# Performance work log

Measured on AMD Instinct MI355X. Metric: run time of the kernel, lower is better.

Reference implementation:

```python
import jax, jax.numpy as jnp
import numpy as np

PROJ_SCALE = 0.1


def setup_inputs() -> dict:
    key = jax.random.key(0)
    ks = jax.random.split(key, 6)
    B, D, K, E = 8192, 256, 63, 64  # batch, n_features, num_breakpoints, emb_dim_per_feature
    x_num = jax.random.normal(ks[0], (B, D), dtype=jnp.float32)
    basis_weight = jax.random.normal(ks[1], (D, K + 1, E), dtype=jnp.float32) * 0.001
    basis_bias = jnp.zeros((D, E), dtype=jnp.float32)
    proj_w = jax.random.normal(ks[2], (D, D * E), dtype=jnp.float32) * 0.01  # torch Linear weight (out, in)
    proj_b = jnp.zeros((D,), dtype=jnp.float32)
    breakpoint_min = jax.random.normal(ks[3], (D, 1), dtype=jnp.float32) * 0.1
    breakpoint_delta_raw = jax.random.normal(ks[4], (D, K), dtype=jnp.float32) * 0.5
    return {
        "x_num": x_num,
        "basis_weight": basis_weight,
        "basis_bias": basis_bias,
        "proj_w": proj_w,
        "proj_b": proj_b,
        "breakpoint_min": breakpoint_min,
        "breakpoint_delta_raw": breakpoint_delta_raw,
    }


def reference(x_num, basis_weight, basis_bias, proj_w, proj_b, breakpoint_min, breakpoint_delta_raw):
    # breakpoints: monotone via softplus deltas + cumsum, shape [D, K]
    deltas = jax.nn.softplus(breakpoint_delta_raw)
    breakpoints = breakpoint_min + jnp.cumsum(deltas, axis=1)
    # piecewise-linear basis: [B, D, K+1]
    basis = jax.nn.relu(x_num[:, :, None] - breakpoints[None, :, :])
    basis = jnp.concatenate([x_num[:, :, None], basis], axis=-1)
    # per-feature batched matmul: [B, D, E]
    embeddings = jnp.einsum("bdf,dfe->bde", basis, basis_weight) + basis_bias
    flat = embeddings.reshape(x_num.shape[0], -1)  # [B, D*E]
    x_emb = x_num + PROJ_SCALE * (flat @ proj_w.T + proj_b)
    return x_emb, embeddings, breakpoints
```

## Files before the change

kernel.cpp:

```cpp
#include <hip/hip_runtime.h>
#include <hip/hip_bf16.h>

#define NB 8192
#define ND 256
#define NKBP 63
#define NF 64
#define NE 64
#define NKP 16384
#define NDE 16384
#define NSPLIT 4

typedef __attribute__((ext_vector_type(8))) short short8_t;
typedef __attribute__((ext_vector_type(4))) short short4_t;
typedef __attribute__((ext_vector_type(4))) float f32x4;

__device__ __forceinline__ unsigned short bfbits(float v) {
  union { __hip_bfloat16 b; unsigned short u; } cv;
  cv.b = __float2bfloat16(v);
  return cv.u;
}
__device__ __forceinline__ float bf2f(unsigned short s) {
  return __uint_as_float(((unsigned)s) << 16);
}

__global__ void k_maxx(const float* __restrict__ x, float* __restrict__ bmax) {
  const int t = threadIdx.x;
  const float* px = x + (size_t)blockIdx.x * 8192;
  float m = 0.f;
  #pragma unroll 4
  for (int i = t; i < 8192; i += 256) m = fmaxf(m, px[i]);
  #pragma unroll
  for (int off = 32; off > 0; off >>= 1) m = fmaxf(m, __shfl_down(m, off, 64));
  __shared__ float red[4];
  if ((t & 63) == 0) red[t >> 6] = m;
  __syncthreads();
  if (t == 0) bmax[blockIdx.x] = fmaxf(fmaxf(red[0], red[1]), fmaxf(red[2], red[3]));
}

__global__ void k_bp(const float* __restrict__ bmin, const float* __restrict__ draw,
                     const float* __restrict__ bmax, float* __restrict__ obp,
                     int* __restrict__ fdv, int* __restrict__ fcutc,
                     float* __restrict__ thrT) {
  const int d = threadIdx.x;
  __shared__ float mred[256];
  __shared__ int fds[256];
  mred[d] = bmax[d];
  __syncthreads();
  for (int s = 128; s > 0; s >>= 1) {
    if (d < s) mred[d] = fmaxf(mred[d], mred[d + s]);
    __syncthreads();
  }
  const float maxx = mred[0];
  float a = bmin[d];
  int cnt = 0;
  if (thrT) thrT[d * 64] = 0.0f;
  for (int j = 0; j < NKBP; ++j) {
    float r = draw[d * NKBP + j];
    a += fmaxf(r, 0.f) + log1pf(expf(-fabsf(r)));
    obp[d * NKBP + j] = a;
    if (thrT) thrT[d * 64 + 1 + j] = a;
    cnt += (a < maxx) ? 1 : 0;
  }
  const int Fd = 1 + cnt;
  fdv[d] = Fd;
  fds[d] = Fd;
  __syncthreads();
  if (d < NSPLIT) {
    int mx = 0;
    for (int k = 0; k < 64; ++k) mx = max(mx, fds[d * 64 + k]);
    fcutc[d] = (mx > 32) ? 2 : 1;
  }
}

__global__ void k_prep(const float* __restrict__ bw, unsigned short* __restrict__ bwT) {
  const int d = blockIdx.x;
  const int t = threadIdx.x;
  const int f = t >> 2, e0 = (t & 3) * 16;
  const int kf = f >> 5, lg = (f >> 3) & 3, j = f & 7;
  const size_t base = ((((size_t)d * 2 + kf) * 4 + lg) * 64) * 8 + j;
  #pragma unroll
  for (int q = 0; q < 4; ++q) {
    f32x4 v = *(const f32x4*)(bw + (size_t)d * 4096 + f * 64 + e0 + q * 4);
    #pragma unroll
    for (int r = 0; r < 4; ++r)
      bwT[base + (size_t)(e0 + q * 4 + r) * 8] = bfbits(v[r]);
  }
}

__global__ __launch_bounds__(256, 2) void k_w2(
    const float* __restrict__ bw, const float* __restrict__ pw,
    const float* __restrict__ bb, const int* __restrict__ fcutc,
    unsigned short* __restrict__ w2f, float* __restrict__ cb_part) {
  const int d = blockIdx.x;
  const int t = threadIdx.x;
  const int l = t & 63, w = t >> 6;
  const int lr = l & 15, lg = l >> 4;
  const int nkf = fcutc[d >> 6];
  __shared__ unsigned short pwS[256 * 72];
  __shared__ unsigned short bwS[64 * 72];
  __shared__ float bbS[64];

  {
    const int rr = t >> 4, e0 = (t & 15) * 4;
    #pragma unroll
    for (int it = 0; it < 16; ++it) {
      const int n = it * 16 + rr;
      f32x4 v = *(const f32x4*)(pw + (size_t)n * NDE + d * 64 + e0);
      short4_t s;
      s[0] = (short)bfbits(v[0]); s[1] = (short)bfbits(v[1]);
      s[2] = (short)bfbits(v[2]); s[3] = (short)bfbits(v[3]);
      *(short4_t*)(pwS + n * 72 + e0) = s;
    }
    const int itmax = (nkf == 2) ? 4 : 2;
    for (int it = 0; it < itmax; ++it) {
      const int f = it * 16 + rr;
      f32x4 v = *(const f32x4*)(bw + (size_t)d * 4096 + f * 64 + e0);
      short4_t s;
      s[0] = (short)bfbits(v[0]); s[1] = (short)bfbits(v[1]);
      s[2] = (short)bfbits(v[2]); s[3] = (short)bfbits(v[3]);
      *(short4_t*)(bwS + f * 72 + e0) = s;
    }
    if (t < 64) bbS[t] = bb[(size_t)d * 64 + t];
  }
  __syncthreads();

  f32x4 acc[4][4];
  #pragma unroll
  for (int mi = 0; mi < 4; ++mi)
    #pragma unroll
    for (int ni = 0; ni < 4; ++ni) acc[mi][ni] = (f32x4){0.f, 0.f, 0.f, 0.f};

  const int nimax = (nkf == 2) ? 4 : 2;
  for (int kf = 0; kf < nkf; ++kf) {
    short8_t afr[4], bfr[4];
    #pragma unroll
    for (int mi = 0; mi < 4; ++mi) {
      const int n = w * 64 + mi * 16 + lr;
      afr[mi] = *(const short8_t*)(pwS + n * 72 + kf * 32 + lg * 8);
    }
    for (int ni = 0; ni < nimax; ++ni) {
      const int f = ni * 16 + lr;
      bfr[ni] = *(const short8_t*)(bwS + f * 72 + kf * 32 + lg * 8);
    }
    for (int ni = 0; ni < nimax; ++ni)
      #pragma unroll
      for (int mi = 0; mi < 4; ++mi)
        acc[mi][ni] = __builtin_amdgcn_mfma_f32_16x16x32_bf16(afr[mi], bfr[ni], acc[mi][ni], 0, 0, 0);
  }

  #pragma unroll
  for (int mi = 0; mi < 4; ++mi)
    for (int ni = 0; ni < nimax; ++ni) {
      const int kf_s = ni >> 1;
      const int lgp  = (ni * 2 + (lr >> 3)) & 3;
      const int jj   = lr & 7;
      const int nb   = w * 64 + mi * 16 + lg * 4;
      const size_t base = (((size_t)d * 2 + kf_s) * 4 + lgp) * 256;
      #pragma unroll
      for (int r = 0; r < 4; ++r)
        w2f[(base + (nb + r)) * 8 + jj] = bfbits(acc[mi][ni][r]);
    }

  {
    float cacc = 0.f;
    #pragma unroll 8
    for (int e = 0; e < 64; ++e) cacc += bf2f(pwS[t * 72 + e]) * bbS[e];
    cb_part[(size_t)d * 256 + t] = cacc;
  }
}

__global__ void k_cbr(const float* __restrict__ cb_part, float* __restrict__ c) {
  const int t = threadIdx.x;
  float a0 = 0.f, a1 = 0.f, a2 = 0.f, a3 = 0.f;
  for (int d = 0; d < ND; d += 4) {
    a0 += cb_part[(size_t)(d + 0) * 256 + t];
    a1 += cb_part[(size_t)(d + 1) * 256 + t];
    a2 += cb_part[(size_t)(d + 2) * 256 + t];
    a3 += cb_part[(size_t)(d + 3) * 256 + t];
  }
  c[t] = (a0 + a1) + (a2 + a3);
}

template<bool KF1>
__device__ __forceinline__ void proj_kloop(
    const unsigned short* const (&bbase)[4], const float* const (&xrow)[2],
    const float* thrS_lg, bool lg0, f32x4 (&acc)[2][4]) {
  for (int c = 0; c < 8; ++c) {
    f32x4 xqa[2], xqb[2];
    #pragma unroll
    for (int mi = 0; mi < 2; ++mi) {
      xqa[mi] = *(const f32x4*)(xrow[mi] + c * 8);
      xqb[mi] = *(const f32x4*)(xrow[mi] + c * 8 + 4);
    }
    #pragma unroll
    for (int dd = 0; dd < 8; ++dd) {
      const int dl = c * 8 + dd;
      short8_t bfr0[4], bfr1[4];
      #pragma unroll
      for (int ni = 0; ni < 4; ++ni)
        bfr0[ni] = *(const short8_t*)(bbase[ni] + (size_t)dl * 16384);
      if (KF1) {
        #pragma unroll
        for (int ni = 0; ni < 4; ++ni)
          bfr1[ni] = *(const short8_t*)(bbase[ni] + (size_t)dl * 16384 + 8192);
      }
      const float* tp = thrS_lg + dl * 64;
      f32x4 ta = *(const f32x4*)(tp);
      f32x4 tb = *(const f32x4*)(tp + 4);
      short8_t afr0[2], afr1[2];
      #pragma unroll
      for (int mi = 0; mi < 2; ++mi) {
        const float xv = (dd < 4) ? xqa[mi][dd & 3] : xqb[mi][dd & 3];
        short8_t A0;
        A0[0] = (short)bfbits(lg0 ? xv : fmaxf(xv - ta[0], 0.f));
        A0[1] = (short)bfbits(fmaxf(xv - ta[1], 0.f));
        A0[2] = (short)bfbits(fmaxf(xv - ta[2], 0.f));
        A0[3] = (short)bfbits(fmaxf(xv - ta[3], 0.f));
        A0[4] = (short)bfbits(fmaxf(xv - tb[0], 0.f));
        A0[5] = (short)bfbits(fmaxf(xv - tb[1], 0.f));
        A0[6] = (short)bfbits(fmaxf(xv - tb[2], 0.f));
        A0[7] = (short)bfbits(fmaxf(xv - tb[3], 0.f));
        afr0[mi] = A0;
      }
      if (KF1) {
        f32x4 tc = *(const f32x4*)(tp + 32);
        f32x4 td = *(const f32x4*)(tp + 36);
        #pragma unroll
        for (int mi = 0; mi < 2; ++mi) {
          const float xv = (dd < 4) ? xqa[mi][dd & 3] : xqb[mi][dd & 3];
          short8_t A1;
          A1[0] = (short)bfbits(fmaxf(xv - tc[0], 0.f));
          A1[1] = (short)bfbits(fmaxf(xv - tc[1], 0.f));
          A1[2] = (short)bfbits(fmaxf(xv - tc[2], 0.f));
          A1[3] = (short)bfbits(fmaxf(xv - tc[3], 0.f));
          A1[4] = (short)bfbits(fmaxf(xv - td[0], 0.f));
          A1[5] = (short)bfbits(fmaxf(xv - td[1], 0.f));
          A1[6] = (short)bfbits(fmaxf(xv - td[2], 0.f));
          A1[7] = (short)bfbits(fmaxf(xv - td[3], 0.f));
          afr1[mi] = A1;
        }
      }
      #pragma unroll
      for (int mi = 0; mi < 2; ++mi)
        #pragma unroll
        for (int ni = 0; ni < 4; ++ni)
          acc[mi][ni] = __builtin_amdgcn_mfma_f32_16x16x32_bf16(afr0[mi], bfr0[ni], acc[mi][ni], 0, 0, 0);
      if (KF1) {
        #pragma unroll
        for (int mi = 0; mi < 2; ++mi)
          #pragma unroll
          for (int ni = 0; ni < 4; ++ni)
            acc[mi][ni] = __builtin_amdgcn_mfma_f32_16x16x32_bf16(afr1[mi], bfr1[ni], acc[mi][ni], 0, 0, 0);
      }
    }
  }
}

__global__ __launch_bounds__(256, 3) void k_proj(
    const unsigned short* __restrict__ w2f, const float* __restrict__ bp,
    const float* __restrict__ x, const int* __restrict__ fcutc,
    float* __restrict__ pbuf) {
  const int t = threadIdx.x;
  const int l = t & 63, w = t >> 6;
  const int lr = l & 15, lg = l >> 4;
  const int bM = blockIdx.x * 128;
  const int bN = blockIdx.y * 64;
  const int d0 = blockIdx.z * 64;
  __shared__ float thrS[64 * 64];

  for (int i = t; i < 4096; i += 256) {
    const int dl = i >> 6, f = i & 63;
    thrS[i] = (f >= 1) ? bp[(size_t)(d0 + dl) * NKBP + f - 1] : 0.0f;
  }
  __syncthreads();

  f32x4 acc[2][4];
  #pragma unroll
  for (int mi = 0; mi < 2; ++mi)
    #pragma unroll
    for (int ni = 0; ni < 4; ++ni) acc[mi][ni] = (f32x4){0.f, 0.f, 0.f, 0.f};

  const bool lg0 = (lg == 0);
  const unsigned short* bbase[4];
  #pragma unroll
  for (int ni = 0; ni < 4; ++ni)
    bbase[ni] = w2f + (size_t)d0 * 16384 + (size_t)(bN + ni * 16 + lr) * 8 + (size_t)lg * 2048;
  const float* xrow[2];
  #pragma unroll
  for (int mi = 0; mi < 2; ++mi)
    xrow[mi] = x + (size_t)(bM + w * 32 + mi * 16 + lr) * ND + d0;

  const int nkf = fcutc[blockIdx.z];
  if (nkf == 1) proj_kloop<false>(bbase, xrow, thrS + lg * 8, lg0, acc);
  else          proj_kloop<true >(bbase, xrow, thrS + lg * 8, lg0, acc);

  float* pp = pbuf + (size_t)blockIdx.z * ((size_t)NB * ND);
  #pragma unroll
  for (int mi = 0; mi < 2; ++mi)
    #pragma unroll
    for (int ni = 0; ni < 4; ++ni) {
      const int col = bN + ni * 16 + lr;
      const int rowb = bM + w * 32 + mi * 16 + lg * 4;
      #pragma unroll
      for (int r = 0; r < 4; ++r)
        pp[(size_t)(rowb + r) * ND + col] = acc[mi][ni][r];
    }
}

__global__ void k_comb(const float* __restrict__ x, const float* __restrict__ pbuf,
                       const float* __restrict__ cbuf, const float* __restrict__ pb,
                       float* __restrict__ xe) {
  const size_t i = ((size_t)blockIdx.x * 256 + threadIdx.x) * 4;
  const int n = (int)(i & 255);
  f32x4 s = *(const f32x4*)(pbuf + i);
  #pragma unroll
  for (int p = 1; p < NSPLIT; ++p)
    s += *(const f32x4*)(pbuf + (size_t)p * 2097152 + i);
  f32x4 cv = *(const f32x4*)(cbuf + n);
  f32x4 pv = *(const f32x4*)(pb + n);
  f32x4 xv = *(const f32x4*)(x + i);
  *(f32x4*)(xe + i) = xv + 0.1f * (s + cv + pv);
}

__global__ __launch_bounds__(256, 3) void k_emb(
    const float* __restrict__ x, const unsigned short* __restrict__ bwT,
    const float* __restrict__ bb, const float* __restrict__ thrT,
    const int* __restrict__ fdv, float* __restrict__ oe) {
  const int d = blockIdx.x;
  const int b0 = blockIdx.y * 256;
  const int t = threadIdx.x;
  const int l = t & 63, w = t >> 6;
  const int lr = l & 15, lg = l >> 4;
  __shared__ float cS[4 * 32 * 68];

  const int nkf = (fdv[d] > 32) ? 2 : 1;

  float xg[4];
  #pragma unroll
  for (int mi = 0; mi < 4; ++mi)
    xg[mi] = x[(size_t)(b0 + w * 64 + mi * 16 + lr) * ND + d];

  f32x4 ta = *(const f32x4*)(thrT + d * 64 + lg * 8);
  f32x4 tb = *(const f32x4*)(thrT + d * 64 + lg * 8 + 4);
  const bool lg0 = (lg == 0);

  float bbv[4];
  #pragma unroll
  for (int ni = 0; ni < 4; ++ni) bbv[ni] = bb[(size_t)d * 64 + ni * 16 + lr];

  const unsigned short* bk0 = bwT + ((size_t)d * 8 + lg) * 512;
  short8_t bfr0[4];
  #pragma unroll
  for (int ni = 0; ni < 4; ++ni)
    bfr0[ni] = *(const short8_t*)(bk0 + (ni * 16 + lr) * 8);

  short8_t afr0[4];
  #pragma unroll
  for (int mi = 0; mi < 4; ++mi) {
    const float xv = xg[mi];
    short8_t A0;
    A0[0] = (short)bfbits(lg0 ? xv : fmaxf(xv - ta[0], 0.f));
    A0[1] = (short)bfbits(fmaxf(xv - ta[1], 0.f));
    A0[2] = (short)bfbits(fmaxf(xv - ta[2], 0.f));
    A0[3] = (short)bfbits(fmaxf(xv - ta[3], 0.f));
    A0[4] = (short)bfbits(fmaxf(xv - tb[0], 0.f));
    A0[5] = (short)bfbits(fmaxf(xv - tb[1], 0.f));
    A0[6] = (short)bfbits(fmaxf(xv - tb[2], 0.f));
    A0[7] = (short)bfbits(fmaxf(xv - tb[3], 0.f));
    afr0[mi] = A0;
  }

  f32x4 acc[4][4];
  #pragma unroll
  for (int mi = 0; mi < 4; ++mi)
    #pragma unroll
    for (int ni = 0; ni < 4; ++ni) acc[mi][ni] = (f32x4){0.f, 0.f, 0.f, 0.f};
  #pragma unroll
  for (int mi = 0; mi < 4; ++mi)
    #pragma unroll
    for (int ni = 0; ni < 4; ++ni)
      acc[mi][ni] = __builtin_amdgcn_mfma_f32_16x16x32_bf16(afr0[mi], bfr0[ni], acc[mi][ni], 0, 0, 0);

  if (nkf == 2) {
    f32x4 tc = *(const f32x4*)(thrT + d * 64 + 32 + lg * 8);
    f32x4 td = *(const f32x4*)(thrT + d * 64 + 36 + lg * 8);
    const unsigned short* bk1 = bwT + ((size_t)d * 8 + 4 + lg) * 512;
    short8_t afr1[4], bfr1[4];
    #pragma unroll
    for (int ni = 0; ni < 4; ++ni)
      bfr1[ni] = *(const short8_t*)(bk1 + (ni * 16 + lr) * 8);
    #pragma unroll
    for (int mi = 0; mi < 4; ++mi) {
      const float xv = xg[mi];
      short8_t A1;
      A1[0] = (short)bfbits(fmaxf(xv - tc[0], 0.f));
      A1[1] = (short)bfbits(fmaxf(xv - tc[1], 0.f));
      A1[2] = (short)bfbits(fmaxf(xv - tc[2], 0.f));
      A1[3] = (short)bfbits(fmaxf(xv - tc[3], 0.f));
      A1[4] = (short)bfbits(fmaxf(xv - td[0], 0.f));
      A1[5] = (short)bfbits(fmaxf(xv - td[1], 0.f));
      A1[6] = (short)bfbits(fmaxf(xv - td[2], 0.f));
      A1[7] = (short)bfbits(fmaxf(xv - td[3], 0.f));
      afr1[mi] = A1;
    }
    #pragma unroll
    for (int mi = 0; mi < 4; ++mi)
      #pragma unroll
      for (int ni = 0; ni < 4; ++ni)
        acc[mi][ni] = __builtin_amdgcn_mfma_f32_16x16x32_bf16(afr1[mi], bfr1[ni], acc[mi][ni], 0, 0, 0);
  }

  const int rsub = l >> 4;
  const int c4 = (l & 15) * 4;
  #pragma unroll
  for (int half = 0; half < 2; ++half) {
    #pragma unroll
    for (int ni = 0; ni < 4; ++ni) {
      #pragma unroll
      for (int mi = 0; mi < 2; ++mi) {
        const int rw = mi * 16 + lg * 4;
        #pragma unroll
        for (int r = 0; r < 4; ++r)
          cS[w * 2176 + (rw + r) * 68 + ni * 16 + lr] = acc[half * 2 + mi][ni][r] + bbv[ni];
      }
    }
    #pragma unroll
    for (int p = 0; p < 8; ++p) {
      const int rl = p * 4 + rsub;
      f32x4 v = *(const f32x4*)(cS + w * 2176 + rl * 68 + c4);
      *(f32x4*)(oe + (size_t)(b0 + w * 64 + half * 32 + rl) * NDE + d * 64 + c4) = v;
    }
  }
}

__global__ __launch_bounds__(256, 2) void k_emb_fb(
    const float* __restrict__ x, const float* __restrict__ bw,
    const float* __restrict__ bb, const float* __restrict__ bp,
    const int* __restrict__ fdv, float* __restrict__ oe) {
  const int d = blockIdx.x;
  const int b0 = blockIdx.y * 256;
  const int t = threadIdx.x;
  const int l = t & 63, w = t >> 6;
  const int lr = l & 15, lg = l >> 4;
  __shared__ unsigned short btS[64 * 72];
  __shared__ float thrF[64];
  __shared__ float bbS[64];
  __shared__ float cS[4 * 64 * 68];

  const int nkf = (fdv[d] > 32) ? 2 : 1;
  float xg[4];
  #pragma unroll
  for (int mi = 0; mi < 4; ++mi)
    xg[mi] = x[(size_t)(b0 + w * 64 + mi * 16 + lr) * ND + d];

  if (t < 64) thrF[t] = (t >= 1) ? bp[(size_t)d * NKBP + t - 1] : 0.0f;
  else if (t < 128) bbS[t - 64] = bb[(size_t)d * 64 + (t - 64)];
  {
    const float* bwd = bw + (size_t)d * 4096;
    const int f = t >> 2, e0 = (t & 3) * 16;
    #pragma unroll
    for (int q = 0; q < 4; ++q) {
      f32x4 v = *(const f32x4*)(bwd + f * 64 + e0 + q * 4);
      #pragma unroll
      for (int r = 0; r < 4; ++r) {
        const int e = e0 + q * 4 + r;
        btS[e * 72 + f] = bfbits(v[r]);
      }
    }
  }
  __syncthreads();

  f32x4 ta = *(const f32x4*)(thrF + lg * 8);
  f32x4 tb = *(const f32x4*)(thrF + lg * 8 + 4);
  const bool lg0 = (lg == 0);

  short8_t afr0[4];
  #pragma unroll
  for (int mi = 0; mi < 4; ++mi) {
    const float xv = xg[mi];
    short8_t A0;
    A0[0] = (short)bfbits(lg0 ? xv : fmaxf(xv - ta[0], 0.f));
    A0[1] = (short)bfbits(fmaxf(xv - ta[1], 0.f));
    A0[2] = (short)bfbits(fmaxf(xv - ta[2], 0.f));
    A0[3] = (short)bfbits(fmaxf(xv - ta[3], 0.f));
    A0[4] = (short)bfbits(fmaxf(xv - tb[0], 0.f));
    A0[5] = (short)bfbits(fmaxf(xv - tb[1], 0.f));
    A0[6] = (short)bfbits(fmaxf(xv - tb[2], 0.f));
    A0[7] = (short)bfbits(fmaxf(xv - tb[3], 0.f));
    afr0[mi] = A0;
  }
  short8_t bfr0[4];
  #pragma unroll
  for (int ni = 0; ni < 4; ++ni) {
    const int e = ni * 16 + lr;
    bfr0[ni] = *(const short8_t*)(btS + e * 72 + lg * 8);
  }
  f32x4 acc[4][4];
  #pragma unroll
  for (int mi = 0; mi < 4; ++mi)
    #pragma unroll
    for (int ni = 0; ni < 4; ++ni) acc[mi][ni] = (f32x4){0.f, 0.f, 0.f, 0.f};
  #pragma unroll
  for (int mi = 0; mi < 4; ++mi)
    #pragma unroll
    for (int ni = 0; ni < 4; ++ni)
      acc[mi][ni] = __builtin_amdgcn_mfma_f32_16x16x32_bf16(afr0[mi], bfr0[ni], acc[mi][ni], 0, 0, 0);

  if (nkf == 2) {
    f32x4 tc = *(const f32x4*)(thrF + 32 + lg * 8);
    f32x4 td = *(const f32x4*)(thrF + 36 + lg * 8);
    short8_t afr1[4], bfr1[4];
    #pragma unroll
    for (int mi = 0; mi < 4; ++mi) {
      const float xv = xg[mi];
      short8_t A1;
      A1[0] = (short)bfbits(fmaxf(xv - tc[0], 0.f));
      A1[1] = (short)bfbits(fmaxf(xv - tc[1], 0.f));
      A1[2] = (short)bfbits(fmaxf(xv - tc[2], 0.f));
      A1[3] = (short)bfbits(fmaxf(xv - tc[3], 0.f));
      A1[4] = (short)bfbits(fmaxf(xv - td[0], 0.f));
      A1[5] = (short)bfbits(fmaxf(xv - td[1], 0.f));
      A1[6] = (short)bfbits(fmaxf(xv - td[2], 0.f));
      A1[7] = (short)bfbits(fmaxf(xv - td[3], 0.f));
      afr1[mi] = A1;
    }
    #pragma unroll
    for (int ni = 0; ni < 4; ++ni) {
      const int e = ni * 16 + lr;
      bfr1[ni] = *(const short8_t*)(btS + e * 72 + 32 + lg * 8);
    }
    #pragma unroll
    for (int mi = 0; mi < 4; ++mi)
      #pragma unroll
      for (int ni = 0; ni < 4; ++ni)
        acc[mi][ni] = __builtin_amdgcn_mfma_f32_16x16x32_bf16(afr1[mi], bfr1[ni], acc[mi][ni], 0, 0, 0);
  }

  #pragma unroll
  for (int ni = 0; ni < 4; ++ni) {
    const float bbv = bbS[ni * 16 + lr];
    #pragma unroll
    for (int mi = 0; mi < 4; ++mi) {
      const int rw = mi * 16 + lg * 4;
      #pragma unroll
      for (int r = 0; r < 4; ++r)
        cS[w * 4352 + (rw + r) * 68 + ni * 16 + lr] = acc[mi][ni][r] + bbv;
    }
  }
  __syncthreads();

  const int rsub = t >> 4;
  const int c4 = (t & 15) * 4;
  #pragma unroll
  for (int p = 0; p < 16; ++p) {
    const int row = p * 16 + rsub;
    const int wsrc = row >> 6, wr = row & 63;
    f32x4 v = *(const f32x4*)(cS + wsrc * 4352 + wr * 68 + c4);
    *(f32x4*)(oe + (size_t)(b0 + row) * NDE + d * 64 + c4) = v;
  }
}

extern "C" void kernel_launch(void* const* d_in, const int* in_sizes, int n_in,
                              void* d_out, int out_size, void* d_ws, size_t ws_size,
                              hipStream_t stream) {
  const float* x    = (const float*)d_in[0];
  const float* bw   = (const float*)d_in[1];
  const float* bb   = (const float*)d_in[2];
  const float* pw   = (const float*)d_in[3];
  const float* pb   = (const float*)d_in[4];
  const float* bmin = (const float*)d_in[5];
  const float* draw = (const float*)d_in[6];

  float* out    = (float*)d_out;
  float* out_x  = out;
  float* out_e  = out + (size_t)NB * ND;
  float* out_bp = out_e + (size_t)NB * NDE;

  unsigned short* w2f = (unsigned short*)out_x;
  float* cbuf    = out_e;
  float* pbuf    = out_e + 65536;
  float* cb_part = out_e + 65536 + NSPLIT * 2097152;

  float* wsf  = (float*)d_ws;
  float* bmax = wsf;
  int*   fdv  = (int*)wsf + 256;
  int*   fcutc= (int*)wsf + 512;
  float* thrT = wsf + 768;
  unsigned short* bwT = (unsigned short*)(wsf + 768 + 16384);
  const bool FAST = ws_size >= (size_t)(768 + 16384) * 4 + (size_t)2097152 * 2 + 256;

  k_maxx<<<dim3(256),          dim3(256), 0, stream>>>(x, bmax);
  k_bp  <<<dim3(1),            dim3(256), 0, stream>>>(bmin, draw, bmax, out_bp, fdv, fcutc,
                                                       FAST ? thrT : (float*)nullptr);
  if (FAST)
    k_prep<<<dim3(256),        dim3(256), 0, stream>>>(bw, bwT);
  k_w2  <<<dim3(256),          dim3(256), 0, stream>>>(bw, pw, bb, fcutc, w2f, cb_part);
  k_cbr <<<dim3(1),            dim3(256), 0, stream>>>(cb_part, cbuf);
  k_proj<<<dim3(64, 4, NSPLIT),dim3(256), 0, stream>>>(w2f, out_bp, x, fcutc, pbuf);
  k_comb<<<dim3(2048),         dim3(256), 0, stream>>>(x, pbuf, cbuf, pb, out_x);
  if (FAST)
    k_emb <<<dim3(256, 32),    dim3(256), 0, stream>>>(x, bwT, bb, thrT, fdv, out_e);
  else
    k_emb_fb<<<dim3(256, 32),  dim3(256), 0, stream>>>(x, bw, bb, out_bp, fdv, out_e);
}
```

Baseline: 261.5 us.

## Restructure embedding kernel to write full contiguous output rows per batch tile

```diff
diff --git a/kernel.cpp b/kernel.cpp
--- a/kernel.cpp
+++ b/kernel.cpp
@@ -23,6 +23,32 @@
   return __uint_as_float(((unsigned)s) << 16);
 }
 
+__global__ void k_mp(const float* __restrict__ x, const float* __restrict__ bw,
+                     float* __restrict__ bmax, unsigned short* __restrict__ bwT) {
+  const int t = threadIdx.x;
+  const float* px = x + (size_t)blockIdx.x * 8192;
+  float m = 0.f;
+  #pragma unroll 4
+  for (int i = t; i < 8192; i += 256) m = fmaxf(m, px[i]);
+  #pragma unroll
+  for (int off = 32; off > 0; off >>= 1) m = fmaxf(m, __shfl_down(m, off, 64));
+  __shared__ float red[4];
+  if ((t & 63) == 0) red[t >> 6] = m;
+  __syncthreads();
+  if (t == 0) bmax[blockIdx.x] = fmaxf(fmaxf(red[0], red[1]), fmaxf(red[2], red[3]));
+  const int d = blockIdx.x;
+  const int f = t >> 2, e0 = (t & 3) * 16;
+  const int kf = f >> 5, lg = (f >> 3) & 3, j = f & 7;
+  const size_t base = ((((size_t)d * 2 + kf) * 4 + lg) * 64) * 8 + j;
+  #pragma unroll
+  for (int q = 0; q < 4; ++q) {
+    f32x4 v = *(const f32x4*)(bw + (size_t)d * 4096 + f * 64 + e0 + q * 4);
+    #pragma unroll
+    for (int r = 0; r < 4; ++r)
+      bwT[base + (size_t)(e0 + q * 4 + r) * 8] = bfbits(v[r]);
+  }
+}
+
 __global__ void k_maxx(const float* __restrict__ x, float* __restrict__ bmax) {
   const int t = threadIdx.x;
   const float* px = x + (size_t)blockIdx.x * 8192;
@@ -42,9 +68,11 @@
                      int* __restrict__ fdv, int* __restrict__ fcutc,
                      float* __restrict__ thrT) {
   const int d = threadIdx.x;
+  __shared__ float drawS[ND * NKBP];
   __shared__ float mred[256];
   __shared__ int fds[256];
   mred[d] = bmax[d];
+  for (int i = d; i < ND * NKBP; i += 256) drawS[i] = draw[i];
   __syncthreads();
   for (int s = 128; s > 0; s >>= 1) {
     if (d < s) mred[d] = fmaxf(mred[d], mred[d + s]);
@@ -55,7 +83,7 @@
   int cnt = 0;
   if (thrT) thrT[d * 64] = 0.0f;
   for (int j = 0; j < NKBP; ++j) {
-    float r = draw[d * NKBP + j];
+    float r = drawS[d * NKBP + j];
     a += fmaxf(r, 0.f) + log1pf(expf(-fabsf(r)));
     obp[d * NKBP + j] = a;
     if (thrT) thrT[d * 64 + 1 + j] = a;
@@ -69,21 +97,6 @@
     int mx = 0;
     for (int k = 0; k < 64; ++k) mx = max(mx, fds[d * 64 + k]);
     fcutc[d] = (mx > 32) ? 2 : 1;
-  }
-}
-
-__global__ void k_prep(const float* __restrict__ bw, unsigned short* __restrict__ bwT) {
-  const int d = blockIdx.x;
-  const int t = threadIdx.x;
-  const int f = t >> 2, e0 = (t & 3) * 16;
-  const int kf = f >> 5, lg = (f >> 3) & 3, j = f & 7;
-  const size_t base = ((((size_t)d * 2 + kf) * 4 + lg) * 64) * 8 + j;
-  #pragma unroll
-  for (int q = 0; q < 4; ++q) {
-    f32x4 v = *(const f32x4*)(bw + (size_t)d * 4096 + f * 64 + e0 + q * 4);
-    #pragma unroll
-    for (int r = 0; r < 4; ++r)
-      bwT[base + (size_t)(e0 + q * 4 + r) * 8] = bfbits(v[r]);
   }
 }
 
@@ -322,37 +335,131 @@
   *(f32x4*)(xe + i) = xv + 0.1f * (s + cv + pv);
 }
 
-__global__ __launch_bounds__(256, 3) void k_emb(
+__global__ __launch_bounds__(256, 2) void k_emb2(
     const float* __restrict__ x, const unsigned short* __restrict__ bwT,
     const float* __restrict__ bb, const float* __restrict__ thrT,
+    const int* __restrict__ fdv, const int* __restrict__ fcutc,
+    float* __restrict__ oe) {
+  const int b0 = blockIdx.x * 16;
+  const int t = threadIdx.x;
+  const int l = t & 63, w = t >> 6;
+  const int lr = l & 15, lg = l >> 4;
+  __shared__ float xS[16 * 260];
+  __shared__ float thrS[256 * 32];
+  __shared__ float slab[16 * 268];
+
+  {
+    const int r = t >> 4, c16 = (t & 15) * 16;
+    #pragma unroll
+    for (int q = 0; q < 4; ++q) {
+      f32x4 v = *(const f32x4*)(x + (size_t)(b0 + r) * ND + c16 + q * 4);
+      *(f32x4*)(xS + r * 260 + c16 + q * 4) = v;
+    }
+  }
+  for (int i = t; i < 256 * 32; i += 256) {
+    const int dS = i >> 5, f = i & 31;
+    thrS[i] = thrT[dS * 64 + f];
+  }
+  int fc[NSPLIT];
+  #pragma unroll
+  for (int z = 0; z < NSPLIT; ++z) fc[z] = fcutc[z];
+  __syncthreads();
+
+  const bool lg0 = (lg == 0);
+  const int ecol = w * 16 + lr;
+
+  for (int g = 0; g < 64; ++g) {
+    #pragma unroll
+    for (int dd = 0; dd < 4; ++dd) {
+      const int d = g * 4 + dd;
+      f32x4 ta = *(const f32x4*)(thrS + d * 32 + lg * 8);
+      f32x4 tb = *(const f32x4*)(thrS + d * 32 + lg * 8 + 4);
+      const float xv = xS[lr * 260 + d];
+      short8_t A0;
+      A0[0] = (short)bfbits(lg0 ? xv : fmaxf(xv - ta[0], 0.f));
+      A0[1] = (short)bfbits(fmaxf(xv - ta[1], 0.f));
+      A0[2] = (short)bfbits(fmaxf(xv - ta[2], 0.f));
+      A0[3] = (short)bfbits(fmaxf(xv - ta[3], 0.f));
+      A0[4] = (short)bfbits(fmaxf(xv - tb[0], 0.f));
+      A0[5] = (short)bfbits(fmaxf(xv - tb[1], 0.f));
+      A0[6] = (short)bfbits(fmaxf(xv - tb[2], 0.f));
+      A0[7] = (short)bfbits(fmaxf(xv - tb[3], 0.f));
+      short8_t B0 = *(const short8_t*)(bwT + ((size_t)d * 8 + lg) * 512 + ecol * 8);
+      const float bbv = bb[(size_t)d * 64 + ecol];
+      f32x4 acc = (f32x4){0.f, 0.f, 0.f, 0.f};
+      acc = __builtin_amdgcn_mfma_f32_16x16x32_bf16(A0, B0, acc, 0, 0, 0);
+      if (fc[d >> 6] == 2) {
+        if (fdv[d] > 32) {
+          f32x4 tc = *(const f32x4*)(thrT + d * 64 + 32 + lg * 8);
+          f32x4 td = *(const f32x4*)(thrT + d * 64 + 36 + lg * 8);
+          short8_t A1;
+          A1[0] = (short)bfbits(fmaxf(xv - tc[0], 0.f));
+          A1[1] = (short)bfbits(fmaxf(xv - tc[1], 0.f));
+          A1[2] = (short)bfbits(fmaxf(xv - tc[2], 0.f));
+          A1[3] = (short)bfbits(fmaxf(xv - tc[3], 0.f));
+          A1[4] = (short)bfbits(fmaxf(xv - td[0], 0.f));
+          A1[5] = (short)bfbits(fmaxf(xv - td[1], 0.f));
+          A1[6] = (short)bfbits(fmaxf(xv - td[2], 0.f));
+          A1[7] = (short)bfbits(fmaxf(xv - td[3], 0.f));
+          short8_t B1 = *(const short8_t*)(bwT + ((size_t)d * 8 + 4 + lg) * 512 + ecol * 8);
+          acc = __builtin_amdgcn_mfma_f32_16x16x32_bf16(A1, B1, acc, 0, 0, 0);
+        }
+      }
+      #pragma unroll
+      for (int r2 = 0; r2 < 4; ++r2)
+        slab[(lg * 4 + r2) * 268 + dd * 64 + ecol] = acc[r2] + bbv;
+    }
+    __syncthreads();
+    #pragma unroll
+    for (int rr = 0; rr < 4; ++rr) {
+      const int row = w * 4 + rr;
+      f32x4 v = *(const f32x4*)(slab + row * 268 + l * 4);
+      *(f32x4*)(oe + (size_t)(b0 + row) * NDE + g * 256 + l * 4) = v;
+    }
+    __syncthreads();
+  }
+}
+
+__global__ __launch_bounds__(256, 2) void k_emb_fb(
+    const float* __restrict__ x, const float* __restrict__ bw,
+    const float* __restrict__ bb, const float* __restrict__ bp,
     const int* __restrict__ fdv, float* __restrict__ oe) {
   const int d = blockIdx.x;
   const int b0 = blockIdx.y * 256;
   const int t = threadIdx.x;
   const int l = t & 63, w = t >> 6;
   const int lr = l & 15, lg = l >> 4;
-  __shared__ float cS[4 * 32 * 68];
+  __shared__ unsigned short btS[64 * 72];
+  __shared__ float thrF[64];
+  __shared__ float bbS[64];
+  __shared__ float cS[4 * 64 * 68];
 
   const int nkf = (fdv[d] > 32) ? 2 : 1;
-
   float xg[4];
   #pragma unroll
   for (int mi = 0; mi < 4; ++mi)
     xg[mi] = x[(size_t)(b0 + w * 64 + mi * 16 + lr) * ND + d];
 
-  f32x4 ta = *(const f32x4*)(thrT + d * 64 + lg * 8);
-  f32x4 tb = *(const f32x4*)(thrT + d * 64 + lg * 8 + 4);
+  if (t < 64) thrF[t] = (t >= 1) ? bp[(size_t)d * NKBP + t - 1] : 0.0f;
+  else if (t < 128) bbS[t - 64] = bb[(size_t)d * 64 + (t - 64)];
+  {
+    const float* bwd = bw + (size_t)d * 4096;
+    const int f = t >> 2, e0 = (t & 3) * 16;
+    #pragma unroll
+    for (int q = 0; q < 4; ++q) {
+      f32x4 v = *(const f32x4*)(bwd + f * 64 + e0 + q * 4);
+      #pragma unroll
+      for (int r = 0; r < 4; ++r) {
+        const int e = e0 + q * 4 + r;
+        btS[e * 72 + f] = bfbits(v[r]);
+      }
+    }
+  }
+  __syncthreads();
+
+  f32x4 ta = *(const f32x4*)(thrF + lg * 8);
+  f32x4 tb = *(const f32x4*)(thrF + lg * 8 + 4);
   const bool lg0 = (lg == 0);
-
-  float bbv[4];
-  #pragma unroll
-  for (int ni = 0; ni < 4; ++ni) bbv[ni] = bb[(size_t)d * 64 + ni * 16 + lr];
-
-  const unsigned short* bk0 = bwT + ((size_t)d * 8 + lg) * 512;
-  short8_t bfr0[4];
-  #pragma unroll
-  for (int ni = 0; ni < 4; ++ni)
-    bfr0[ni] = *(const short8_t*)(bk0 + (ni * 16 + lr) * 8);
 
   short8_t afr0[4];
   #pragma unroll
@@ -369,7 +476,12 @@
     A0[7] = (short)bfbits(fmaxf(xv - tb[3], 0.f));
     afr0[mi] = A0;
   }
-
+  short8_t bfr0[4];
+  #pragma unroll
+  for (int ni = 0; ni < 4; ++ni) {
+    const int e = ni * 16 + lr;
+    bfr0[ni] = *(const short8_t*)(btS + e * 72 + lg * 8);
+  }
   f32x4 acc[4][4];
   #pragma unroll
   for (int mi = 0; mi < 4; ++mi)
@@ -382,13 +494,9 @@
       acc[mi][ni] = __builtin_amdgcn_mfma_f32_16x16x32_bf16(afr0[mi], bfr0[ni], acc[mi][ni], 0, 0, 0);
 
   if (nkf == 2) {
-    f32x4 tc = *(const f32x4*)(thrT + d * 64 + 32 + lg * 8);
-    f32x4 td = *(const f32x4*)(thrT + d * 64 + 36 + lg * 8);
-    const unsigned short* bk1 = bwT + ((size_t)d * 8 + 4 + lg) * 512;
+    f32x4 tc = *(const f32x4*)(thrF + 32 + lg * 8);
+    f32x4 td = *(const f32x4*)(thrF + 36 + lg * 8);
     short8_t afr1[4], bfr1[4];
-    #pragma unroll
-    for (int ni = 0; ni < 4; ++ni)
-      bfr1[ni] = *(const short8_t*)(bk1 + (ni * 16 + lr) * 8);
     #pragma unroll
     for (int mi = 0; mi < 4; ++mi) {
       const float xv = xg[mi];
@@ -404,127 +512,6 @@
       afr1[mi] = A1;
     }
     #pragma unroll
-    for (int mi = 0; mi < 4; ++mi)
-      #pragma unroll
-      for (int ni = 0; ni < 4; ++ni)
-        acc[mi][ni] = __builtin_amdgcn_mfma_f32_16x16x32_bf16(afr1[mi], bfr1[ni], acc[mi][ni], 0, 0, 0);
-  }
-
-  const int rsub = l >> 4;
-  const int c4 = (l & 15) * 4;
-  #pragma unroll
-  for (int half = 0; half < 2; ++half) {
-    #pragma unroll
-    for (int ni = 0; ni < 4; ++ni) {
-      #pragma unroll
-      for (int mi = 0; mi < 2; ++mi) {
-        const int rw = mi * 16 + lg * 4;
-        #pragma unroll
-        for (int r = 0; r < 4; ++r)
-          cS[w * 2176 + (rw + r) * 68 + ni * 16 + lr] = acc[half * 2 + mi][ni][r] + bbv[ni];
-      }
-    }
-    #pragma unroll
-    for (int p = 0; p < 8; ++p) {
-      const int rl = p * 4 + rsub;
-      f32x4 v = *(const f32x4*)(cS + w * 2176 + rl * 68 + c4);
-      *(f32x4*)(oe + (size_t)(b0 + w * 64 + half * 32 + rl) * NDE + d * 64 + c4) = v;
-    }
-  }
-}
-
-__global__ __launch_bounds__(256, 2) void k_emb_fb(
-    const float* __restrict__ x, const float* __restrict__ bw,
-    const float* __restrict__ bb, const float* __restrict__ bp,
-    const int* __restrict__ fdv, float* __restrict__ oe) {
-  const int d = blockIdx.x;
-  const int b0 = blockIdx.y * 256;
-  const int t = threadIdx.x;
-  const int l = t & 63, w = t >> 6;
-  const int lr = l & 15, lg = l >> 4;
-  __shared__ unsigned short btS[64 * 72];
-  __shared__ float thrF[64];
-  __shared__ float bbS[64];
-  __shared__ float cS[4 * 64 * 68];
-
-  const int nkf = (fdv[d] > 32) ? 2 : 1;
-  float xg[4];
-  #pragma unroll
-  for (int mi = 0; mi < 4; ++mi)
-    xg[mi] = x[(size_t)(b0 + w * 64 + mi * 16 + lr) * ND + d];
-
-  if (t < 64) thrF[t] = (t >= 1) ? bp[(size_t)d * NKBP + t - 1] : 0.0f;
-  else if (t < 128) bbS[t - 64] = bb[(size_t)d * 64 + (t - 64)];
-  {
-    const float* bwd = bw + (size_t)d * 4096;
-    const int f = t >> 2, e0 = (t & 3) * 16;
-    #pragma unroll
-    for (int q = 0; q < 4; ++q) {
-      f32x4 v = *(const f32x4*)(bwd + f * 64 + e0 + q * 4);
-      #pragma unroll
-      for (int r = 0; r < 4; ++r) {
-        const int e = e0 + q * 4 + r;
-        btS[e * 72 + f] = bfbits(v[r]);
-      }
-    }
-  }
-  __syncthreads();
-
-  f32x4 ta = *(const f32x4*)(thrF + lg * 8);
-  f32x4 tb = *(const f32x4*)(thrF + lg * 8 + 4);
-  const bool lg0 = (lg == 0);
-
-  short8_t afr0[4];
-  #pragma unroll
-  for (int mi = 0; mi < 4; ++mi) {
-    const float xv = xg[mi];
-    short8_t A0;
-    A0[0] = (short)bfbits(lg0 ? xv : fmaxf(xv - ta[0], 0.f));
-    A0[1] = (short)bfbits(fmaxf(xv - ta[1], 0.f));
-    A0[2] = (short)bfbits(fmaxf(xv - ta[2], 0.f));
-    A0[3] = (short)bfbits(fmaxf(xv - ta[3], 0.f));
-    A0[4] = (short)bfbits(fmaxf(xv - tb[0], 0.f));
-    A0[5] = (short)bfbits(fmaxf(xv - tb[1], 0.f));
-    A0[6] = (short)bfbits(fmaxf(xv - tb[2], 0.f));
-    A0[7] = (short)bfbits(fmaxf(xv - tb[3], 0.f));
-    afr0[mi] = A0;
-  }
-  short8_t bfr0[4];
-  #pragma unroll
-  for (int ni = 0; ni < 4; ++ni) {
-    const int e = ni * 16 + lr;
-    bfr0[ni] = *(const short8_t*)(btS + e * 72 + lg * 8);
-  }
-  f32x4 acc[4][4];
-  #pragma unroll
-  for (int mi = 0; mi < 4; ++mi)
-    #pragma unroll
-    for (int ni = 0; ni < 4; ++ni) acc[mi][ni] = (f32x4){0.f, 0.f, 0.f, 0.f};
-  #pragma unroll
-  for (int mi = 0; mi < 4; ++mi)
-    #pragma unroll
-    for (int ni = 0; ni < 4; ++ni)
-      acc[mi][ni] = __builtin_amdgcn_mfma_f32_16x16x32_bf16(afr0[mi], bfr0[ni], acc[mi][ni], 0, 0, 0);
-
-  if (nkf == 2) {
-    f32x4 tc = *(const f32x4*)(thrF + 32 + lg * 8);
-    f32x4 td = *(const f32x4*)(thrF + 36 + lg * 8);
-    short8_t afr1[4], bfr1[4];
-    #pragma unroll
-    for (int mi = 0; mi < 4; ++mi) {
-      const float xv = xg[mi];
-      short8_t A1;
-      A1[0] = (short)bfbits(fmaxf(xv - tc[0], 0.f));
-      A1[1] = (short)bfbits(fmaxf(xv - tc[1], 0.f));
-      A1[2] = (short)bfbits(fmaxf(xv - tc[2], 0.f));
-      A1[3] = (short)bfbits(fmaxf(xv - tc[3], 0.f));
-      A1[4] = (short)bfbits(fmaxf(xv - td[0], 0.f));
-      A1[5] = (short)bfbits(fmaxf(xv - td[1], 0.f));
-      A1[6] = (short)bfbits(fmaxf(xv - td[2], 0.f));
-      A1[7] = (short)bfbits(fmaxf(xv - td[3], 0.f));
-      afr1[mi] = A1;
-    }
-    #pragma unroll
     for (int ni = 0; ni < 4; ++ni) {
       const int e = ni * 16 + lr;
       bfr1[ni] = *(const short8_t*)(btS + e * 72 + 32 + lg * 8);
@@ -589,17 +576,18 @@
   unsigned short* bwT = (unsigned short*)(wsf + 768 + 16384);
   const bool FAST = ws_size >= (size_t)(768 + 16384) * 4 + (size_t)2097152 * 2 + 256;
 
-  k_maxx<<<dim3(256),          dim3(256), 0, stream>>>(x, bmax);
+  if (FAST)
+    k_mp <<<dim3(256),         dim3(256), 0, stream>>>(x, bw, bmax, bwT);
+  else
+    k_maxx<<<dim3(256),        dim3(256), 0, stream>>>(x, bmax);
   k_bp  <<<dim3(1),            dim3(256), 0, stream>>>(bmin, draw, bmax, out_bp, fdv, fcutc,
                                                        FAST ? thrT : (float*)nullptr);
-  if (FAST)
-    k_prep<<<dim3(256),        dim3(256), 0, stream>>>(bw, bwT);
   k_w2  <<<dim3(256),          dim3(256), 0, stream>>>(bw, pw, bb, fcutc, w2f, cb_part);
   k_cbr <<<dim3(1),            dim3(256), 0, stream>>>(cb_part, cbuf);
   k_proj<<<dim3(64, 4, NSPLIT),dim3(256), 0, stream>>>(w2f, out_bp, x, fcutc, pbuf);
   k_comb<<<dim3(2048),         dim3(256), 0, stream>>>(x, pbuf, cbuf, pb, out_x);
   if (FAST)
-    k_emb <<<dim3(256, 32),    dim3(256), 0, stream>>>(x, bwT, bb, thrT, fdv, out_e);
+    k_emb2<<<dim3(512),        dim3(256), 0, stream>>>(x, bwT, bb, thrT, fdv, fcutc, out_e);
   else
     k_emb_fb<<<dim3(256, 32),  dim3(256), 0, stream>>>(x, bw, bb, out_bp, fdv, out_e);
 }
```

Result: slower. 335.4 us (+28.2%).

## Fuse max/prep kernels, stage breakpoint raws in LDS, retile embedding store

Applied to the files above, without the earlier changes.

```diff
diff --git a/kernel.cpp b/kernel.cpp
--- a/kernel.cpp
+++ b/kernel.cpp
@@ -23,6 +23,32 @@
   return __uint_as_float(((unsigned)s) << 16);
 }
 
+__global__ void k_mp(const float* __restrict__ x, const float* __restrict__ bw,
+                     float* __restrict__ bmax, unsigned short* __restrict__ bwT) {
+  const int t = threadIdx.x;
+  const float* px = x + (size_t)blockIdx.x * 8192;
+  float m = 0.f;
+  #pragma unroll 4
+  for (int i = t; i < 8192; i += 256) m = fmaxf(m, px[i]);
+  #pragma unroll
+  for (int off = 32; off > 0; off >>= 1) m = fmaxf(m, __shfl_down(m, off, 64));
+  __shared__ float red[4];
+  if ((t & 63) == 0) red[t >> 6] = m;
+  __syncthreads();
+  if (t == 0) bmax[blockIdx.x] = fmaxf(fmaxf(red[0], red[1]), fmaxf(red[2], red[3]));
+  const int d = blockIdx.x;
+  const int f = t >> 2, e0 = (t & 3) * 16;
+  const int kf = f >> 5, lg = (f >> 3) & 3, j = f & 7;
+  const size_t base = ((((size_t)d * 2 + kf) * 4 + lg) * 64) * 8 + j;
+  #pragma unroll
+  for (int q = 0; q < 4; ++q) {
+    f32x4 v = *(const f32x4*)(bw + (size_t)d * 4096 + f * 64 + e0 + q * 4);
+    #pragma unroll
+    for (int r = 0; r < 4; ++r)
+      bwT[base + (size_t)(e0 + q * 4 + r) * 8] = bfbits(v[r]);
+  }
+}
+
 __global__ void k_maxx(const float* __restrict__ x, float* __restrict__ bmax) {
   const int t = threadIdx.x;
   const float* px = x + (size_t)blockIdx.x * 8192;
@@ -42,9 +68,11 @@
                      int* __restrict__ fdv, int* __restrict__ fcutc,
                      float* __restrict__ thrT) {
   const int d = threadIdx.x;
+  __shared__ float drawS[ND * NKBP];
   __shared__ float mred[256];
   __shared__ int fds[256];
   mred[d] = bmax[d];
+  for (int i = d; i < ND * NKBP; i += 256) drawS[i] = draw[i];
   __syncthreads();
   for (int s = 128; s > 0; s >>= 1) {
     if (d < s) mred[d] = fmaxf(mred[d], mred[d + s]);
@@ -55,7 +83,7 @@
   int cnt = 0;
   if (thrT) thrT[d * 64] = 0.0f;
   for (int j = 0; j < NKBP; ++j) {
-    float r = draw[d * NKBP + j];
+    float r = drawS[d * NKBP + j];
     a += fmaxf(r, 0.f) + log1pf(expf(-fabsf(r)));
     obp[d * NKBP + j] = a;
     if (thrT) thrT[d * 64 + 1 + j] = a;
@@ -69,21 +97,6 @@
     int mx = 0;
     for (int k = 0; k < 64; ++k) mx = max(mx, fds[d * 64 + k]);
     fcutc[d] = (mx > 32) ? 2 : 1;
-  }
-}
-
-__global__ void k_prep(const float* __restrict__ bw, unsigned short* __restrict__ bwT) {
-  const int d = blockIdx.x;
-  const int t = threadIdx.x;
-  const int f = t >> 2, e0 = (t & 3) * 16;
-  const int kf = f >> 5, lg = (f >> 3) & 3, j = f & 7;
-  const size_t base = ((((size_t)d * 2 + kf) * 4 + lg) * 64) * 8 + j;
-  #pragma unroll
-  for (int q = 0; q < 4; ++q) {
-    f32x4 v = *(const f32x4*)(bw + (size_t)d * 4096 + f * 64 + e0 + q * 4);
-    #pragma unroll
-    for (int r = 0; r < 4; ++r)
-      bwT[base + (size_t)(e0 + q * 4 + r) * 8] = bfbits(v[r]);
   }
 }
 
@@ -322,23 +335,23 @@
   *(f32x4*)(xe + i) = xv + 0.1f * (s + cv + pv);
 }
 
-__global__ __launch_bounds__(256, 3) void k_emb(
+__global__ __launch_bounds__(256, 3) void k_emb3(
     const float* __restrict__ x, const unsigned short* __restrict__ bwT,
     const float* __restrict__ bb, const float* __restrict__ thrT,
     const int* __restrict__ fdv, float* __restrict__ oe) {
-  const int d = blockIdx.x;
-  const int b0 = blockIdx.y * 256;
+  const int dc = blockIdx.x;
+  const int b0 = blockIdx.y * 32;
   const int t = threadIdx.x;
   const int l = t & 63, w = t >> 6;
   const int lr = l & 15, lg = l >> 4;
-  __shared__ float cS[4 * 32 * 68];
+  const int d = dc * 4 + w;
+  __shared__ float slab[32 * 260];
 
   const int nkf = (fdv[d] > 32) ? 2 : 1;
 
-  float xg[4];
-  #pragma unroll
-  for (int mi = 0; mi < 4; ++mi)
-    xg[mi] = x[(size_t)(b0 + w * 64 + mi * 16 + lr) * ND + d];
+  float xg[2];
+  xg[0] = x[(size_t)(b0 + lr) * ND + d];
+  xg[1] = x[(size_t)(b0 + 16 + lr) * ND + d];
 
   f32x4 ta = *(const f32x4*)(thrT + d * 64 + lg * 8);
   f32x4 tb = *(const f32x4*)(thrT + d * 64 + lg * 8 + 4);
@@ -354,9 +367,9 @@
   for (int ni = 0; ni < 4; ++ni)
     bfr0[ni] = *(const short8_t*)(bk0 + (ni * 16 + lr) * 8);
 
-  short8_t afr0[4];
-  #pragma unroll
-  for (int mi = 0; mi < 4; ++mi) {
+  short8_t afr0[2];
+  #pragma unroll
+  for (int mi = 0; mi < 2; ++mi) {
     const float xv = xg[mi];
     short8_t A0;
     A0[0] = (short)bfbits(lg0 ? xv : fmaxf(xv - ta[0], 0.f));
@@ -370,13 +383,13 @@
     afr0[mi] = A0;
   }
 
-  f32x4 acc[4][4];
-  #pragma unroll
-  for (int mi = 0; mi < 4; ++mi)
+  f32x4 acc[2][4];
+  #pragma unroll
+  for (int mi = 0; mi < 2; ++mi)
     #pragma unroll
     for (int ni = 0; ni < 4; ++ni) acc[mi][ni] = (f32x4){0.f, 0.f, 0.f, 0.f};
   #pragma unroll
-  for (int mi = 0; mi < 4; ++mi)
+  for (int mi = 0; mi < 2; ++mi)
     #pragma unroll
     for (int ni = 0; ni < 4; ++ni)
       acc[mi][ni] = __builtin_amdgcn_mfma_f32_16x16x32_bf16(afr0[mi], bfr0[ni], acc[mi][ni], 0, 0, 0);
@@ -385,12 +398,12 @@
     f32x4 tc = *(const f32x4*)(thrT + d * 64 + 32 + lg * 8);
     f32x4 td = *(const f32x4*)(thrT + d * 64 + 36 + lg * 8);
     const unsigned short* bk1 = bwT + ((size_t)d * 8 + 4 + lg) * 512;
-    short8_t afr1[4], bfr1[4];
+    short8_t afr1[2], bfr1[4];
     #pragma unroll
     for (int ni = 0; ni < 4; ++ni)
       bfr1[ni] = *(const short8_t*)(bk1 + (ni * 16 + lr) * 8);
     #pragma unroll
-    for (int mi = 0; mi < 4; ++mi) {
+    for (int mi = 0; mi < 2; ++mi) {
       const float xv = xg[mi];
       short8_t A1;
       A1[0] = (short)bfbits(fmaxf(xv - tc[0], 0.f));
@@ -404,32 +417,26 @@
       afr1[mi] = A1;
     }
     #pragma unroll
-    for (int mi = 0; mi < 4; ++mi)
+    for (int mi = 0; mi < 2; ++mi)
       #pragma unroll
       for (int ni = 0; ni < 4; ++ni)
         acc[mi][ni] = __builtin_amdgcn_mfma_f32_16x16x32_bf16(afr1[mi], bfr1[ni], acc[mi][ni], 0, 0, 0);
   }
 
-  const int rsub = l >> 4;
-  const int c4 = (l & 15) * 4;
-  #pragma unroll
-  for (int half = 0; half < 2; ++half) {
-    #pragma unroll
-    for (int ni = 0; ni < 4; ++ni) {
-      #pragma unroll
-      for (int mi = 0; mi < 2; ++mi) {
-        const int rw = mi * 16 + lg * 4;
-        #pragma unroll
-        for (int r = 0; r < 4; ++r)
-          cS[w * 2176 + (rw + r) * 68 + ni * 16 + lr] = acc[half * 2 + mi][ni][r] + bbv[ni];
-      }
-    }
-    #pragma unroll
-    for (int p = 0; p < 8; ++p) {
-      const int rl = p * 4 + rsub;
-      f32x4 v = *(const f32x4*)(cS + w * 2176 + rl * 68 + c4);
-      *(f32x4*)(oe + (size_t)(b0 + w * 64 + half * 32 + rl) * NDE + d * 64 + c4) = v;
-    }
+  #pragma unroll
+  for (int ni = 0; ni < 4; ++ni)
+    #pragma unroll
+    for (int mi = 0; mi < 2; ++mi)
+      #pragma unroll
+      for (int r = 0; r < 4; ++r)
+        slab[(mi * 16 + lg * 4 + r) * 260 + w * 64 + ni * 16 + lr] = acc[mi][ni][r] + bbv[ni];
+  __syncthreads();
+
+  #pragma unroll
+  for (int p = 0; p < 8; ++p) {
+    const int row = w * 8 + p;
+    f32x4 v = *(const f32x4*)(slab + row * 260 + l * 4);
+    *(f32x4*)(oe + (size_t)(b0 + row) * NDE + dc * 256 + l * 4) = v;
   }
 }
 
@@ -589,17 +596,18 @@
   unsigned short* bwT = (unsigned short*)(wsf + 768 + 16384);
   const bool FAST = ws_size >= (size_t)(768 + 16384) * 4 + (size_t)2097152 * 2 + 256;
 
-  k_maxx<<<dim3(256),          dim3(256), 0, stream>>>(x, bmax);
+  if (FAST)
+    k_mp <<<dim3(256),         dim3(256), 0, stream>>>(x, bw, bmax, bwT);
+  else
+    k_maxx<<<dim3(256),        dim3(256), 0, stream>>>(x, bmax);
   k_bp  <<<dim3(1),            dim3(256), 0, stream>>>(bmin, draw, bmax, out_bp, fdv, fcutc,
                                                        FAST ? thrT : (float*)nullptr);
-  if (FAST)
-    k_prep<<<dim3(256),        dim3(256), 0, stream>>>(bw, bwT);
   k_w2  <<<dim3(256),          dim3(256), 0, stream>>>(bw, pw, bb, fcutc, w2f, cb_part);
   k_cbr <<<dim3(1),            dim3(256), 0, stream>>>(cb_part, cbuf);
   k_proj<<<dim3(64, 4, NSPLIT),dim3(256), 0, stream>>>(w2f, out_bp, x, fcutc, pbuf);
   k_comb<<<dim3(2048),         dim3(256), 0, stream>>>(x, pbuf, cbuf, pb, out_x);
   if (FAST)
-    k_emb <<<dim3(256, 32),    dim3(256), 0, stream>>>(x, bwT, bb, thrT, fdv, out_e);
+    k_emb3<<<dim3(64, 256),    dim3(256), 0, stream>>>(x, bwT, bb, thrT, fdv, out_e);
   else
     k_emb_fb<<<dim3(256, 32),  dim3(256), 0, stream>>>(x, bw, bb, out_bp, fdv, out_e);
 }
```

Measured after the change: 235.9 us, median of 2. -9.8%, faster.
